# Optimization experiments

Measured on AMD Instinct MI355X. Metric: run time of the kernel, lower is better.

The kernel has to match this reference:

```python
import jax, jax.numpy as jnp
import numpy as np
from jax import lax

IN_CH = 64
OUT_CH = 64
K = 3
CW = 2 * IN_CH + 49  # in_ch_weight = 2*in_ch + MAX_DISPLACEMENT**2 = 177
B = 8


def setup_inputs() -> dict:
    key = jax.random.key(0)
    ks = jax.random.split(key, 14)
    f = lambda k, s, sc: jax.random.normal(k, s, dtype=jnp.float32) * sc
    he5 = lambda cin: (2.0 / (cin * 25)) ** 0.5
    he3 = lambda cin: (2.0 / (cin * 9)) ** 0.5
    return {
        "x0": f(ks[0], (B, IN_CH, 128, 160), 1.0),
        "y0": f(ks[1], (B, IN_CH, 128, 160), 1.0),
        "x": f(ks[2], (B, IN_CH, 64, 80), 1.0),
        "y": f(ks[3], (B, IN_CH, 64, 80), 1.0),
        # weight-branch 0 (outputs CW channels)
        "w1a": f(ks[4], (IN_CH, CW, 5, 5), he5(CW)),
        "w1b": f(ks[5], (IN_CH, IN_CH, 5, 5), he5(IN_CH)),
        "w1c": f(ks[6], (CW, IN_CH, 3, 3), he3(IN_CH)),
        # weight-branch 1 / final (outputs OUT_CH channels)
        "w2a": f(ks[7], (IN_CH, CW, 5, 5), he5(CW)),
        "w2b": f(ks[8], (IN_CH, IN_CH, 5, 5), he5(IN_CH)),
        "w2c": f(ks[9], (OUT_CH, IN_CH, 3, 3), he3(IN_CH)),
        # grouped 1x1 dynamic-weight generators (per-channel affine maps)
        "wx_w": f(ks[10], (CW, CW * K * K), 0.05),
        "wx_b": f(ks[11], (CW, CW * K * K), 0.05),
        "wxf_w": f(ks[12], (OUT_CH, OUT_CH * K * K), 0.05),
        "wxf_b": f(ks[13], (OUT_CH, OUT_CH * K * K), 0.05),
    }


def _conv(x, w, stride, pad):
    return lax.conv_general_dilated(
        x, w, (stride, stride), [(pad, pad), (pad, pad)],
        dimension_numbers=("NCHW", "OIHW", "NCHW"))


def _pool2(x):
    b, c, h, w = x.shape
    return x.reshape(b, c, h // 2, 2, w // 2, 2).mean(axis=(3, 5))


def _corr(x0, y0):
    # FlowNet-style correlation: max_displacement=7, stride2=2 ->
    # displacements {-6,-4,-2,0,2,4,6}^2 = 49 channels; mean over C.
    b, c, h, w = x0.shape
    D = 6
    yp = jnp.pad(y0, ((0, 0), (0, 0), (D, D), (D, D)))
    outs = []
    for dy in range(-6, 7, 2):
        for dx in range(-6, 7, 2):
            ys = yp[:, :, D + dy:D + dy + h, D + dx:D + dx + w]
            outs.append(jnp.mean(x0 * ys, axis=1))
    return jnp.stack(outs, axis=1)  # [B, 49, H, W]


def _branch(feat, wa, wb, wc):
    h = jax.nn.relu(_conv(feat, wa, 2, 2))
    h = jax.nn.relu(_conv(h, wb, 2, 2))
    h = _conv(h, wc, 2, 1)
    return h.mean(axis=(2, 3))  # adaptive_avg_pool2d -> (1,1), squeezed: [B, Cout]


def _adaptive_conv(x, w, pad):
    # per-sample conv weights w: [B, Cout, Cin, k, k]
    def one(xb, wb):
        return _conv(xb[None], wb, 1, pad)[0]
    return jax.vmap(one)(x, w)


def reference(x0, y0, x, y, w1a, w1b, w1c, w2a, w2b, w2c, wx_w, wx_b, wxf_w, wxf_b):
    b = x.shape[0]
    x0p = _pool2(x0)
    y0p = _pool2(y0)
    corr = _corr(x0p, y0p)                      # [B, 49, H, W]
    feat = jnp.concatenate([corr, x, y], axis=1)  # [B, CW, H, W]

    # iteration 0 (N-1 = 1): generate per-sample [CW,CW,3,3] filters, apply
    fv = _branch(feat, w1a, w1b, w1c)           # [B, CW]
    wx = (fv[:, :, None] * wx_w[None] + wx_b[None]).reshape(b, CW, CW, K, K)
    feat = jax.nn.relu(_adaptive_conv(feat, wx, K // 2))

    # final: generate per-sample [OUT_CH,OUT_CH,3,3] filters and return them
    fv = _branch(feat, w2a, w2b, w2c)           # [B, OUT_CH]
    wxf = (fv[:, :, None] * wxf_w[None] + wxf_b[None]).reshape(b, OUT_CH, OUT_CH, K, K)
    return wxf
```

## Files before the change

kernel.cpp:

```cpp
#include <hip/hip_runtime.h>

typedef unsigned short u16;
typedef __attribute__((ext_vector_type(8))) short bf16x8;
typedef __attribute__((ext_vector_type(4))) float f32x4;
typedef _Float16 half2_t __attribute__((ext_vector_type(2)));

static constexpr int B  = 8;
static constexpr int C  = 64;
static constexpr int CW = 177;
static constexpr int H  = 64, W  = 80;
static constexpr int HP = 68, WP = 84, KC = 192;
static constexpr int PB = HP * WP * KC;
static constexpr int HA = 36, WA = 44;

__device__ __forceinline__ u16 f2b(float f) {
  union { float f; unsigned u; } v; v.f = f;
  unsigned u = v.u;
  return (u16)((u + 0x7FFF + ((u >> 16) & 1)) >> 16);
}
__device__ __forceinline__ u16 f2h(float f) {
  union { _Float16 h; u16 u; } v; v.h = (_Float16)f; return v.u;
}
__device__ __forceinline__ half2_t h2(unsigned u) {
  union { unsigned u; half2_t h; } v; v.u = u; return v.h;
}
__device__ __forceinline__ float blo(unsigned u) {
  union { unsigned v; float f; } t; t.v = u << 16; return t.f;
}
__device__ __forceinline__ float bhi(unsigned u) {
  union { unsigned v; float f; } t; t.v = u & 0xffff0000u; return t.f;
}
__device__ __forceinline__ unsigned pk2(u16 a, u16 b) {
  return (unsigned)a | ((unsigned)b << 16);
}

__global__ __launch_bounds__(256) void setup_pool(
    const float* __restrict__ x0, const float* __restrict__ y0,
    u16* __restrict__ xpT, u16* __restrict__ ypT,
    const float* __restrict__ w1a, const float* __restrict__ w2a,
    const float* __restrict__ w1b, const float* __restrict__ w2b,
    u16* __restrict__ A5a, u16* __restrict__ A5b,
    u16* __restrict__ A5b1, u16* __restrict__ A5b2,
    u16* __restrict__ featP1, u16* __restrict__ haP, u16* __restrict__ featP2) {
  __shared__ u16 lt[80][66];
  int blk0 = blockIdx.x;
  int tid = threadIdx.x;
  if (blk0 < 1024) {
    int sel = blk0 & 1; int h = (blk0 >> 1) & 63; int b = blk0 >> 7;
    const float* in = sel ? y0 : x0;
    u16* out = sel ? ypT : xpT;
#pragma unroll
    for (int i = 0; i < 20; ++i) {
      int e = i * 256 + tid;
      int c = e / 80, w = e % 80;
      const float* p = in + ((size_t)(b * 64 + c) * 128 + 2 * h) * 160 + 2 * w;
      float2 r0 = *(const float2*)p;
      float2 r1 = *(const float2*)(p + 160);
      lt[w][c] = f2h(0.25f * (r0.x + r0.y + r1.x + r1.y));
    }
    __syncthreads();
#pragma unroll
    for (int i = 0; i < 20; ++i) {
      int e = i * 256 + tid;
      int w = e / 64, c = e % 64;
      out[((size_t)(b * H + h) * W + w) * C + c] = lt[w][c];
    }
    return;
  }
  int idx = (blk0 - 1024) * 256 + tid;
  const int n0r = (B * PB) / 8;
  const int n1r = (B * HA * WA * 64) / 8;
  const int n2r = B * 592 * 24;
  const int s1 = 25 * 64 * 192, s2 = 25 * 64 * 64;
  bf16x8 z = 0;
  if (idx < n0r) { ((bf16x8*)featP1)[idx] = z; return; }
  idx -= n0r;
  if (idx < n1r) { ((bf16x8*)haP)[idx] = z; return; }
  idx -= n1r;
  if (idx < n2r) {
    int ch = idx % 24; int pi = (idx / 24) % 592; int b = idx / (24 * 592);
    int row, col;
    if (pi < 336) { int rr = pi / 84; row = (rr < 2) ? rr : rr + 64; col = pi % 84; }
    else { int pj = pi - 336; row = 2 + (pj >> 2); int cc = pj & 3; col = (cc < 2) ? cc : cc + 80; }
    *(bf16x8*)(featP2 + ((size_t)(b * HP + row) * WP + col) * KC + ch * 8) = z;
    return;
  }
  idx -= n2r;
  if (idx < 2 * s1) {
    const float* w = idx < s1 ? w1a : w2a; u16* A = idx < s1 ? A5a : A5b;
    int e = idx % s1;
    int j = e % 192; int i = (e / 192) % 64; int kk = e / (192 * 64);
    int ky = kk / 5, kx = kk % 5;
    float v = (j < CW) ? w[(((size_t)i * CW + j) * 5 + ky) * 5 + kx] : 0.f;
    A[e] = f2b(v);
    return;
  }
  idx -= 2 * s1;
  if (idx < 2 * s2) {
    const float* w = idx < s2 ? w1b : w2b; u16* A = idx < s2 ? A5b1 : A5b2;
    int e = idx % s2;
    int j = e % 64; int i = (e / 64) % 64; int kk = e / (64 * 64);
    int ky = kk / 5, kx = kk % 5;
    A[e] = f2b(w[(((size_t)i * 64 + j) * 5 + ky) * 5 + kx]);
  }
}

__global__ __launch_bounds__(256) void corr_copy(
    const u16* __restrict__ xpT, const u16* __restrict__ ypT,
    const float* __restrict__ x, const float* __restrict__ y,
    u16* __restrict__ featP) {
  __shared__ char sm[40960];
  int blk0 = blockIdx.x;
  int tid = threadIdx.x;
  if (blk0 < 512) {
    int b = blk0 & 7; int h = blk0 >> 3;
    const u16* yb = ypT + (size_t)b * (H * W * C);
    uint4 xv[8];
    {
      const u16* xb = xpT + (((size_t)b * H + h) * W + (tid % 80)) * C;
#pragma unroll
      for (int s = 0; s < 8; ++s) xv[s] = *(const uint4*)(xb + s * 8);
    }
    int w = tid % 80; int og = tid / 80;
    u16* dst = featP + ((size_t)(b * HP + h + 2) * WP + (w + 2)) * KC;
#pragma unroll
    for (int ph = 0; ph < 2; ++ph) {
      const int nrows = ph ? 3 : 4;
      const int nch = nrows * 640;
      if (ph) __syncthreads();
      for (int it = 0; it * 256 + tid < nch; ++it) {
        int idx = it * 256 + tid;
        int row = idx / 640; int rem = idx - row * 640; int q = rem >> 3; int slot = rem & 7;
        int hh = h - 6 + 2 * (ph * 4 + row);
        bf16x8 v = 0;
        if (hh >= 0 && hh < H) v = *(const bf16x8*)(yb + ((size_t)hh * W + q) * C + slot * 8);
        int byte = (idx * 16) ^ ((q & 7) << 4);
        *(bf16x8*)(sm + byte) = v;
      }
      __syncthreads();
      if (tid < 240) {
        const int base = ph ? 28 : 0;
        const int cnt = ph ? 7 : 10;
        const int bound = ph ? 49 : 28;
#pragma unroll
        for (int oi = 0; oi < 10; ++oi) {
          if (oi >= cnt) break;
          int o = base + og * cnt + oi;
          if (o < bound) {
            int rr = o / 7; int dx = (o % 7) * 2 - 6;
            int lr = rr - ph * 4;
            int ww = w + dx;
            float s = 0.f;
            if (ww >= 0 && ww < W) {
#pragma unroll
              for (int sl = 0; sl < 8; ++sl) {
                int byte = (((lr * 640) + ww * 8 + sl) * 16) ^ ((ww & 7) << 4);
                uint4 yv = *(const uint4*)(sm + byte);
                s = __builtin_amdgcn_fdot2(h2(xv[sl].x), h2(yv.x), s, false);
                s = __builtin_amdgcn_fdot2(h2(xv[sl].y), h2(yv.y), s, false);
                s = __builtin_amdgcn_fdot2(h2(xv[sl].z), h2(yv.z), s, false);
                s = __builtin_amdgcn_fdot2(h2(xv[sl].w), h2(yv.w), s, false);
              }
            }
            dst[o] = f2b(s * (1.0f / 64.0f));
          }
        }
      }
    }
    return;
  }
  int blk = blk0 - 512;
  float (*lt)[129] = (float(*)[129])sm;
  int half = blk & 1; int h = (blk >> 1) & 63; int b = blk >> 7;
#pragma unroll
  for (int i = 0; i < 20; ++i) {
    int e = i * 256 + tid;
    int c2 = e / 40, w = e % 40;
    const float* src = (c2 < 64) ? x : y;
    int c = c2 & 63;
    lt[w][c2] = src[((size_t)(b * 64 + c) * H + h) * W + half * 40 + w];
  }
  __syncthreads();
#pragma unroll
  for (int i = 0; i < 20; ++i) {
    int e = i * 256 + tid;
    int wr = e / 128, c = e % 128;
    featP[((size_t)(b * HP + h + 2) * WP + (half * 40 + wr + 2)) * KC + 49 + c] = f2b(lt[wr][c]);
  }
}

__global__ void wx_pack(const float* __restrict__ fv, const float* __restrict__ ww,
                        const float* __restrict__ wb, u16* __restrict__ Apk) {
  int idx = blockIdx.x * blockDim.x + threadIdx.x;
  if (idx >= 9 * 192 * 24) return;
  int j8 = idx % 24; int i = (idx / 24) % 192; int kk = idx / (24 * 192);
  float wwv[8], wbv[8];
#pragma unroll
  for (int jj = 0; jj < 8; ++jj) {
    int j = j8 * 8 + jj;
    if (i < CW && j < CW) {
      size_t o = ((size_t)i * CW + j) * 9 + kk;
      wwv[jj] = ww[o]; wbv[jj] = wb[o];
    } else { wwv[jj] = 0.f; wbv[jj] = 0.f; }
  }
  int rb = i >> 4, il = i & 15;
  int c = j8 >> 3, rem = j8 & 7, half = rem >> 2, kqq = rem & 3;
  size_t dst = (((((size_t)kk * 12 + rb) * 3 + c) * 2 + half) * 64 + kqq * 16 + il) * 8;
  for (int b = 0; b < B; ++b) {
    float f = (i < CW) ? fv[b * CW + i] : 0.f;
    u16 o[8];
#pragma unroll
    for (int jj = 0; jj < 8; ++jj) o[jj] = f2b(f * wwv[jj] + wbv[jj]);
    uint4 v; v.x = pk2(o[0], o[1]); v.y = pk2(o[2], o[3]); v.z = pk2(o[4], o[5]); v.w = pk2(o[6], o[7]);
    *(uint4*)(Apk + (size_t)b * 331776 + dst) = v;
  }
}

__global__ __launch_bounds__(256, 2) void ad_conv_kernel(
    const u16* __restrict__ Apk, const u16* __restrict__ featP, u16* __restrict__ outP) {
  __shared__ u16 lds[2][84 * 64];
  int bid = (int)(blockIdx.x % 8) * 64 + (int)(blockIdx.x / 8);
  int h = bid & 63; int b = bid >> 6;
  int tid = threadIdx.x;
  int lane = tid & 63; int wm = tid >> 6;
  int l15 = lane & 15, kq = lane >> 4;

  f32x4 acc[3][5];
#pragma unroll
  for (int i = 0; i < 3; ++i)
#pragma unroll
    for (int j = 0; j < 5; ++j) acc[i][j] = (f32x4){0.f, 0.f, 0.f, 0.f};

  const u16* fb = featP + (size_t)b * PB;
  const u16* Ab = Apk + (size_t)b * 331776 + (size_t)lane * 8;

  int i0 = tid, i1 = tid + 256, i2 = tid + 512;
  int q0 = i0 >> 3, s0 = i0 & 7;
  int q1 = i1 >> 3, s1 = i1 & 7;
  int q2 = i2 >> 3, s2 = i2 & 7;
  int w0 = (i0 * 16) ^ ((q0 & 7) << 4);
  int w1 = (i1 * 16) ^ ((q1 & 7) << 4);
  int w2 = (i2 * 16) ^ ((q2 & 7) << 4);
  bool a2 = i2 < 672;

  bf16x8 r0, r1, r2;
  {
    const u16* g = fb + ((size_t)(h + 1) * WP) * KC;
    r0 = *(const bf16x8*)(g + (size_t)q0 * KC + s0 * 8);
    r1 = *(const bf16x8*)(g + (size_t)q1 * KC + s1 * 8);
    if (a2) r2 = *(const bf16x8*)(g + (size_t)q2 * KC + s2 * 8);
    char* lw = (char*)lds[0];
    *(bf16x8*)(lw + w0) = r0;
    *(bf16x8*)(lw + w1) = r1;
    if (a2) *(bf16x8*)(lw + w2) = r2;
  }
  __syncthreads();

#pragma unroll
  for (int s = 0; s < 9; ++s) {
    const int c = s / 3, ty = s % 3;
    if (s < 8) {
      const int cn = (s + 1) / 3, tyn = (s + 1) % 3;
      const u16* g = fb + ((size_t)(h + 1 + tyn) * WP) * KC + cn * 64;
      r0 = *(const bf16x8*)(g + (size_t)q0 * KC + s0 * 8);
      r1 = *(const bf16x8*)(g + (size_t)q1 * KC + s1 * 8);
      if (a2) r2 = *(const bf16x8*)(g + (size_t)q2 * KC + s2 * 8);
    }
    const char* lb = (const char*)lds[s & 1];
#pragma unroll
    for (int tx = 0; tx < 3; ++tx) {
      const int tap = ty * 3 + tx;
#pragma unroll
      for (int hk = 0; hk < 2; ++hk) {
        bf16x8 av[3], bv[5];
#pragma unroll
        for (int fm = 0; fm < 3; ++fm)
          av[fm] = *(const bf16x8*)(Ab + (size_t)(((tap * 12 + wm * 3 + fm) * 3 + c) * 2 + hk) * 512);
#pragma unroll
        for (int fn = 0; fn < 5; ++fn) {
          int q = fn * 16 + l15 + tx + 1;
          int byte = ((q * 8 + hk * 4 + kq) * 16) ^ ((q & 7) << 4);
          bv[fn] = *(const bf16x8*)(lb + byte);
        }
        __builtin_amdgcn_s_setprio(1);
#pragma unroll
        for (int fm = 0; fm < 3; ++fm)
#pragma unroll
          for (int fn = 0; fn < 5; ++fn)
            acc[fm][fn] = __builtin_amdgcn_mfma_f32_16x16x32_bf16(av[fm], bv[fn], acc[fm][fn], 0, 0, 0);
        __builtin_amdgcn_s_setprio(0);
      }
    }
    if (s < 8) {
      char* lw = (char*)lds[(s + 1) & 1];
      *(bf16x8*)(lw + w0) = r0;
      *(bf16x8*)(lw + w1) = r1;
      if (a2) *(bf16x8*)(lw + w2) = r2;
      __syncthreads();
    }
  }

#pragma unroll
  for (int fm = 0; fm < 3; ++fm) {
    int i0r = wm * 48 + fm * 16 + kq * 4;
#pragma unroll
    for (int fn = 0; fn < 5; ++fn) {
      int ow = fn * 16 + l15;
      u16* dst = outP + ((size_t)(b * HP + h + 2) * WP + (ow + 2)) * KC + i0r;
      uint2 pkv;
      pkv.x = pk2(f2b(fmaxf(acc[fm][fn][0], 0.f)), f2b(fmaxf(acc[fm][fn][1], 0.f)));
      pkv.y = pk2(f2b(fmaxf(acc[fm][fn][2], 0.f)), f2b(fmaxf(acc[fm][fn][3], 0.f)));
      *(uint2*)dst = pkv;
    }
  }
}

__global__ __launch_bounds__(128, 3) void conv5_split_kernel(
    const u16* __restrict__ A5, const u16* __restrict__ featP, u16* __restrict__ pa) {
  __shared__ u16 lds[2][84 * 64];
  int bid = (int)(blockIdx.x % 8) * 160 + (int)(blockIdx.x / 8);
  int rp = bid % 16; int ty = (bid / 16) % 5; int csel = (bid / 80) % 2; int b = bid / 160;
  int r0 = rp * 2;
  int kc0 = csel * 3;
  int tid = threadIdx.x;
  int lane = tid & 63; int wm = tid >> 6;
  int l15 = lane & 15, kq = lane >> 4;

  f32x4 acc[2][5];
#pragma unroll
  for (int i = 0; i < 2; ++i)
#pragma unroll
    for (int j = 0; j < 5; ++j) acc[i][j] = (f32x4){0.f, 0.f, 0.f, 0.f};

  const u16* fb = featP + (size_t)b * PB;
  int rowg0 = 2 * r0 + ty;

  bf16x8 r[6];
  auto load_chunk = [&](int kc) {
#pragma unroll
    for (int it = 0; it < 6; ++it) {
      int idx = it * 128 + tid;
      if (idx < 672) {
        int slot = idx & 3; int q = (idx >> 2) % 84; int row = idx / 336;
        r[it] = *(const bf16x8*)(fb + ((size_t)(rowg0 + 2 * row) * WP + q) * KC + kc * 32 + slot * 8);
      }
    }
  };
  auto write_chunk = [&](int buf) {
    char* lw = (char*)lds[buf];
#pragma unroll
    for (int it = 0; it < 6; ++it) {
      int idx = it * 128 + tid;
      if (idx < 672) {
        int q = (idx >> 2) % 84;
        int byte = (idx * 16) ^ ((q & 7) << 4);
        *(bf16x8*)(lw + byte) = r[it];
      }
    }
  };

  load_chunk(kc0);
  write_chunk(0);
  __syncthreads();

#pragma unroll
  for (int k = 0; k < 3; ++k) {
    int kc = kc0 + k;
    if (k < 2) load_chunk(kc + 1);
    const char* lb = (const char*)lds[k & 1];
#pragma unroll
    for (int tx = 0; tx < 5; ++tx) {
      bf16x8 av[2], bv[5];
#pragma unroll
      for (int fm = 0; fm < 2; ++fm)
        av[fm] = *(const bf16x8*)(A5 + ((size_t)((ty * 5 + tx) * 64 + wm * 32 + fm * 16 + l15)) * 192 + kc * 32 + kq * 8);
#pragma unroll
      for (int fn = 0; fn < 5; ++fn) {
        int p = fn * 16 + l15;
        int orow = p / 40, ocol = p % 40;
        int q = ocol * 2 + tx;
        int byte = (((orow * 84 + q) * 4 + kq) * 16) ^ ((q & 7) << 4);
        bv[fn] = *(const bf16x8*)(lb + byte);
      }
      __builtin_amdgcn_s_setprio(1);
#pragma unroll
      for (int fm = 0; fm < 2; ++fm)
#pragma unroll
        for (int fn = 0; fn < 5; ++fn)
          acc[fm][fn] = __builtin_amdgcn_mfma_f32_16x16x32_bf16(av[fm], bv[fn], acc[fm][fn], 0, 0, 0);
      __builtin_amdgcn_s_setprio(0);
    }
    if (k < 2) {
      write_chunk((k + 1) & 1);
      __syncthreads();
    }
  }
  int slot10 = csel * 5 + ty;
#pragma unroll
  for (int fm = 0; fm < 2; ++fm) {
    int oc0 = wm * 32 + fm * 16 + kq * 4;
#pragma unroll
    for (int fn = 0; fn < 5; ++fn) {
      int p = fn * 16 + l15;
      int orow = r0 + p / 40, ocol = p % 40;
      u16* dst = pa + (((((size_t)slot10 * B + b) * 32 + orow) * 40 + ocol) * 64) + oc0;
      uint2 pkv;
      pkv.x = pk2(f2b(acc[fm][fn][0]), f2b(acc[fm][fn][1]));
      pkv.y = pk2(f2b(acc[fm][fn][2]), f2b(acc[fm][fn][3]));
      *(uint2*)dst = pkv;
    }
  }
}

__global__ void combine10(const u16* __restrict__ pa, u16* __restrict__ haP) {
  int idx = blockIdx.x * blockDim.x + threadIdx.x;
  if (idx >= B * 32 * 40 * 8) return;
  int c8 = idx & 7; int t = idx >> 3;
  int ocol = t % 40; t /= 40; int orow = t % 32; int b = t / 32;
  float s[8];
#pragma unroll
  for (int k = 0; k < 8; ++k) s[k] = 0.f;
#pragma unroll
  for (int sl = 0; sl < 10; ++sl) {
    const u16* p = pa + ((((size_t)sl * B + b) * 32 + orow) * 40 + ocol) * 64 + c8 * 8;
    uint4 v = *(const uint4*)p;
    s[0] += blo(v.x); s[1] += bhi(v.x); s[2] += blo(v.y); s[3] += bhi(v.y);
    s[4] += blo(v.z); s[5] += bhi(v.z); s[6] += blo(v.w); s[7] += bhi(v.w);
  }
  uint4 o;
  o.x = pk2(f2b(fmaxf(s[0], 0.f)), f2b(fmaxf(s[1], 0.f)));
  o.y = pk2(f2b(fmaxf(s[2], 0.f)), f2b(fmaxf(s[3], 0.f)));
  o.z = pk2(f2b(fmaxf(s[4], 0.f)), f2b(fmaxf(s[5], 0.f)));
  o.w = pk2(f2b(fmaxf(s[6], 0.f)), f2b(fmaxf(s[7], 0.f)));
  *(uint4*)(haP + ((size_t)(b * HA + orow + 2) * WA + (ocol + 2)) * 64 + c8 * 8) = o;
}

template<int TY, int TX, int S, int OH, int OW, int M, int BM, int BN, int POFF,
         int KCIN, int HPIN, int WPIN>
__global__ __launch_bounds__(256) void gemm_conv(
    const u16* __restrict__ A, const u16* __restrict__ featP,
    float* __restrict__ outF, int MT, int NT) {
  constexpr int WM = BM / 2, WN = BN / 2, FM = WM / 16, FN = WN / 16;
  constexpr int NKC = KCIN / 32;
  int nwg = gridDim.x;
  int bid = (int)(blockIdx.x % 8) * (nwg / 8) + (int)(blockIdx.x / 8);
  int mt = bid % MT; int rest = bid / MT; int nt = rest % NT; int b = rest / NT;
  int lane = threadIdx.x & 63; int wv = threadIdx.x >> 6;
  int wm = wv >> 1, wn = wv & 1;
  int l15 = lane & 15, kq = lane >> 4;

  f32x4 acc[FM][FN];
#pragma unroll
  for (int i = 0; i < FM; ++i)
#pragma unroll
    for (int j = 0; j < FN; ++j) acc[i][j] = (f32x4){0.f, 0.f, 0.f, 0.f};

  const u16* Abase = A + (size_t)(mt * BM + wm * WM + l15) * KCIN + kq * 8;
  const u16* fb = featP + (size_t)b * (HPIN * WPIN * KCIN) + kq * 8;

  int ohh[FN], oww[FN];
#pragma unroll
  for (int fn = 0; fn < FN; ++fn) {
    int p = nt * BN + wn * WN + fn * 16 + l15;
    ohh[fn] = p / OW; oww[fn] = p % OW;
  }

  for (int kc = 0; kc < NKC; ++kc) {
    for (int ty = 0; ty < TY; ++ty)
      for (int tx = 0; tx < TX; ++tx) {
        const u16* At = Abase + (size_t)((ty * TX + tx) * M) * KCIN + kc * 32;
        bf16x8 av[FM], bv[FN];
#pragma unroll
        for (int fm = 0; fm < FM; ++fm)
          av[fm] = *(const bf16x8*)(At + fm * 16 * KCIN);
#pragma unroll
        for (int fn = 0; fn < FN; ++fn) {
          int hi = ohh[fn] * S + ty + POFF;
          int wi = oww[fn] * S + tx + POFF;
          bv[fn] = *(const bf16x8*)(fb + (size_t)(hi * WPIN + wi) * KCIN + kc * 32);
        }
#pragma unroll
        for (int fm = 0; fm < FM; ++fm)
#pragma unroll
          for (int fn = 0; fn < FN; ++fn)
            acc[fm][fn] = __builtin_amdgcn_mfma_f32_16x16x32_bf16(av[fm], bv[fn], acc[fm][fn], 0, 0, 0);
      }
  }

#pragma unroll
  for (int fm = 0; fm < FM; ++fm) {
    int oc0 = mt * BM + wm * WM + fm * 16 + kq * 4;
#pragma unroll
    for (int fn = 0; fn < FN; ++fn) {
#pragma unroll
      for (int r = 0; r < 4; ++r) {
        float v = fmaxf(acc[fm][fn][r], 0.f);
        outF[(((size_t)b * M + oc0 + r) * OH + ohh[fn]) * OW + oww[fn]] = v;
      }
    }
  }
}

__global__ void tapsum_kernel(const float* __restrict__ hb, float* __restrict__ Sm) {
  int b = blockIdx.x >> 6; int ic = blockIdx.x & 63; int lane = threadIdx.x;
  const float* p = hb + ((size_t)(b * 64 + ic)) * 320;
  float s[9];
#pragma unroll
  for (int t = 0; t < 9; ++t) s[t] = 0.f;
  for (int i = lane; i < 320; i += 64) {
    int ih = i / 20, iw = i % 20;
    float v = p[i];
#pragma unroll
    for (int ky = 0; ky < 3; ++ky) {
      int t2 = ih + 1 - ky;
      if (t2 < 0 || t2 > 14 || (t2 & 1)) continue;
#pragma unroll
      for (int kx = 0; kx < 3; ++kx) {
        int t3 = iw + 1 - kx;
        if (t3 < 0 || t3 > 18 || (t3 & 1)) continue;
        s[ky * 3 + kx] += v;
      }
    }
  }
#pragma unroll
  for (int t = 0; t < 9; ++t)
#pragma unroll
    for (int off = 32; off > 0; off >>= 1) s[t] += __shfl_down(s[t], off);
  if (lane == 0) {
#pragma unroll
    for (int t = 0; t < 9; ++t) Sm[(b * 64 + ic) * 9 + t] = s[t];
  }
}

__global__ void gemv_fv(const float* __restrict__ w3, const float* __restrict__ Sm,
                        float* __restrict__ fv, int OC) {
  int o = blockIdx.x % OC; int b = blockIdx.x / OC; int lane = threadIdx.x;
  const float* wp = w3 + ((size_t)o * 64 + lane) * 9;
  const float* sp = Sm + ((size_t)b * 64 + lane) * 9;
  float acc = 0.f;
#pragma unroll
  for (int t = 0; t < 9; ++t) acc += wp[t] * sp[t];
#pragma unroll
  for (int off = 32; off > 0; off >>= 1) acc += __shfl_down(acc, off);
  if (lane == 0) fv[b * OC + o] = acc * (1.0f / 80.0f);
}

__global__ void gemv_final(const float* __restrict__ w3, const float* __restrict__ Sm,
                           const float* __restrict__ ww, const float* __restrict__ wb,
                           float* __restrict__ out) {
  int o = blockIdx.x & 63; int b = blockIdx.x >> 6; int lane = threadIdx.x;
  const float* wp = w3 + ((size_t)o * 64 + lane) * 9;
  const float* sp = Sm + ((size_t)b * 64 + lane) * 9;
  float acc = 0.f;
#pragma unroll
  for (int t = 0; t < 9; ++t) acc += wp[t] * sp[t];
#pragma unroll
  for (int off = 32; off > 0; off >>= 1) acc += __shfl_down(acc, off);
  float fvv = __shfl(acc, 0) * (1.0f / 80.0f);
  const float* wwp = ww + (size_t)o * 576;
  const float* wbp = wb + (size_t)o * 576;
  float* op = out + ((size_t)(b * 64 + o)) * 576;
#pragma unroll
  for (int k = 0; k < 9; ++k)
    op[k * 64 + lane] = fvv * wwp[k * 64 + lane] + wbp[k * 64 + lane];
}

extern "C" void kernel_launch(void* const* d_in, const int* in_sizes, int n_in,
                              void* d_out, int out_size, void* d_ws, size_t ws_size,
                              hipStream_t stream) {
  const float* x0    = (const float*)d_in[0];
  const float* y0    = (const float*)d_in[1];
  const float* x     = (const float*)d_in[2];
  const float* y     = (const float*)d_in[3];
  const float* w1a   = (const float*)d_in[4];
  const float* w1b   = (const float*)d_in[5];
  const float* w1c   = (const float*)d_in[6];
  const float* w2a   = (const float*)d_in[7];
  const float* w2b   = (const float*)d_in[8];
  const float* w2c   = (const float*)d_in[9];
  const float* wx_w  = (const float*)d_in[10];
  const float* wx_b  = (const float*)d_in[11];
  const float* wxf_w = (const float*)d_in[12];
  const float* wxf_b = (const float*)d_in[13];
  float* out = (float*)d_out;

  char* base = (char*)d_ws;
  size_t off = 0;
  auto take = [&](size_t bytes) -> char* {
    char* p = base + off; off += (bytes + 255) & ~(size_t)255; return p;
  };
  u16*   featP1 = (u16*)take((size_t)B * PB * 2);
  u16*   featP2 = (u16*)take((size_t)B * PB * 2);
  u16*   paAwx  = (u16*)take((size_t)10 * B * 32 * 40 * 64 * 2);
  u16*   pa     = paAwx;
  u16*   Apk    = paAwx;
  u16*   xpT    = paAwx;
  u16*   ypT    = paAwx + (size_t)B * H * W * C;
  u16*   A5a    = (u16*)take((size_t)25 * 64 * 192 * 2);
  u16*   A5b    = (u16*)take((size_t)25 * 64 * 192 * 2);
  u16*   A5b1   = (u16*)take((size_t)25 * 64 * 64 * 2);
  u16*   A5b2   = (u16*)take((size_t)25 * 64 * 64 * 2);
  u16*   haP    = (u16*)take((size_t)B * HA * WA * 64 * 2);
  float* hb     = (float*)take((size_t)B * 64 * 320 * 4);
  float* Sm     = (float*)take((size_t)B * 64 * 9 * 4);
  float* fv1    = (float*)take((size_t)B * CW * 4);
  if (off > ws_size) return;

  const int TB = 256;

  {
    int nsetup = (B * PB) / 8 + (B * HA * WA * 64) / 8 + B * 592 * 24
               + 2 * 25 * 64 * 192 + 2 * 25 * 64 * 64;
    int grid = 1024 + (nsetup + TB - 1) / TB;
    setup_pool<<<grid, TB, 0, stream>>>(x0, y0, xpT, ypT,
        w1a, w2a, w1b, w2b, A5a, A5b, A5b1, A5b2, featP1, haP, featP2);
  }
  corr_copy<<<512 + 1024, TB, 0, stream>>>(xpT, ypT, x, y, featP1);

  conv5_split_kernel<<<1280, 128, 0, stream>>>(A5a, featP1, pa);
  combine10<<<(B * 32 * 40 * 8 + TB - 1) / TB, TB, 0, stream>>>(pa, haP);
  gemm_conv<5, 5, 2, 16, 20, 64, 32, 32, 0, 64, HA, WA>
      <<<160, TB, 0, stream>>>(A5b1, haP, hb, 2, 10);
  tapsum_kernel<<<B * 64, 64, 0, stream>>>(hb, Sm);
  gemv_fv<<<B * CW, 64, 0, stream>>>(w1c, Sm, fv1, CW);

  wx_pack<<<(9 * 192 * 24 + TB - 1) / TB, TB, 0, stream>>>(fv1, wx_w, wx_b, Apk);
  ad_conv_kernel<<<64 * B, 256, 0, stream>>>(Apk, featP1, featP2);

  conv5_split_kernel<<<1280, 128, 0, stream>>>(A5b, featP2, pa);
  combine10<<<(B * 32 * 40 * 8 + TB - 1) / TB, TB, 0, stream>>>(pa, haP);
  gemm_conv<5, 5, 2, 16, 20, 64, 32, 32, 0, 64, HA, WA>
      <<<160, TB, 0, stream>>>(A5b2, haP, hb, 2, 10);
  tapsum_kernel<<<B * 64, 64, 0, stream>>>(hb, Sm);
  gemv_final<<<B * 64, 64, 0, stream>>>(w2c, Sm, wxf_w, wxf_b, out);
}
```

Baseline: 172.7 us.

## Pre-pack conv weights in MFMA fragment order and stage three rows per chunk

Setup now writes the 5x5 conv weights in a fragment-packed layout, so each lane loads its MFMA A-operand as one contiguous 16-byte slice. The adaptive conv now stages all three input rows of a 64-channel chunk into LDS at once, giving 3 sync stages instead of 9, at the cost of a larger LDS footprint. The generic gemm_conv template is replaced by a specialized conv5b kernel using the packed weights. The larger LDS use may reduce occupancy of the adaptive conv.

```diff
diff --git a/kernel.cpp b/kernel.cpp
--- a/kernel.cpp
+++ b/kernel.cpp
@@ -92,7 +92,9 @@
     int j = e % 192; int i = (e / 192) % 64; int kk = e / (192 * 64);
     int ky = kk / 5, kx = kk % 5;
     float v = (j < CW) ? w[(((size_t)i * CW + j) * 5 + ky) * 5 + kx] : 0.f;
-    A[e] = f2b(v);
+    int rg = i >> 4, l15 = i & 15;
+    int kc = j >> 5, r = j & 31, kq = r >> 3, s = r & 7;
+    A[(((size_t)(kk * 4 + rg) * 6 + kc) * 64 + kq * 16 + l15) * 8 + s] = f2b(v);
     return;
   }
   idx -= 2 * s1;
@@ -101,7 +103,10 @@
     int e = idx % s2;
     int j = e % 64; int i = (e / 64) % 64; int kk = e / (64 * 64);
     int ky = kk / 5, kx = kk % 5;
-    A[e] = f2b(w[(((size_t)i * 64 + j) * 5 + ky) * 5 + kx]);
+    float v = w[(((size_t)i * 64 + j) * 5 + ky) * 5 + kx];
+    int rg = i >> 4, l15 = i & 15;
+    int kc = j >> 5, r = j & 31, kq = r >> 3, s = r & 7;
+    A[(((size_t)(kk * 4 + rg) * 2 + kc) * 64 + kq * 16 + l15) * 8 + s] = f2b(v);
   }
 }
 
@@ -218,7 +223,7 @@
 
 __global__ __launch_bounds__(256, 2) void ad_conv_kernel(
     const u16* __restrict__ Apk, const u16* __restrict__ featP, u16* __restrict__ outP) {
-  __shared__ u16 lds[2][84 * 64];
+  __shared__ u16 lds[2][3 * 84 * 64];
   int bid = (int)(blockIdx.x % 8) * 64 + (int)(blockIdx.x / 8);
   int h = bid & 63; int b = bid >> 6;
   int tid = threadIdx.x;
@@ -234,68 +239,67 @@
   const u16* fb = featP + (size_t)b * PB;
   const u16* Ab = Apk + (size_t)b * 331776 + (size_t)lane * 8;
 
-  int i0 = tid, i1 = tid + 256, i2 = tid + 512;
-  int q0 = i0 >> 3, s0 = i0 & 7;
-  int q1 = i1 >> 3, s1 = i1 & 7;
-  int q2 = i2 >> 3, s2 = i2 & 7;
-  int w0 = (i0 * 16) ^ ((q0 & 7) << 4);
-  int w1 = (i1 * 16) ^ ((q1 & 7) << 4);
-  int w2 = (i2 * 16) ^ ((q2 & 7) << 4);
-  bool a2 = i2 < 672;
-
-  bf16x8 r0, r1, r2;
-  {
-    const u16* g = fb + ((size_t)(h + 1) * WP) * KC;
-    r0 = *(const bf16x8*)(g + (size_t)q0 * KC + s0 * 8);
-    r1 = *(const bf16x8*)(g + (size_t)q1 * KC + s1 * 8);
-    if (a2) r2 = *(const bf16x8*)(g + (size_t)q2 * KC + s2 * 8);
-    char* lw = (char*)lds[0];
-    *(bf16x8*)(lw + w0) = r0;
-    *(bf16x8*)(lw + w1) = r1;
-    if (a2) *(bf16x8*)(lw + w2) = r2;
-  }
+  bf16x8 r[8];
+  auto load_c = [&](int c) {
+#pragma unroll
+    for (int it = 0; it < 8; ++it) {
+      int idx = it * 256 + tid;
+      if (idx < 2016) {
+        int row = idx / 672; int rem = idx - row * 672; int q = rem >> 3; int slot = rem & 7;
+        r[it] = *(const bf16x8*)(fb + ((size_t)(h + 1 + row) * WP + q) * KC + c * 64 + slot * 8);
+      }
+    }
+  };
+  auto write_c = [&](int buf) {
+    char* lw = (char*)lds[buf];
+#pragma unroll
+    for (int it = 0; it < 8; ++it) {
+      int idx = it * 256 + tid;
+      if (idx < 2016) {
+        int q = (idx % 672) >> 3;
+        int byte = (idx * 16) ^ ((q & 7) << 4);
+        *(bf16x8*)(lw + byte) = r[it];
+      }
+    }
+  };
+
+  load_c(0);
+  write_c(0);
   __syncthreads();
 
 #pragma unroll
-  for (int s = 0; s < 9; ++s) {
-    const int c = s / 3, ty = s % 3;
-    if (s < 8) {
-      const int cn = (s + 1) / 3, tyn = (s + 1) % 3;
-      const u16* g = fb + ((size_t)(h + 1 + tyn) * WP) * KC + cn * 64;
-      r0 = *(const bf16x8*)(g + (size_t)q0 * KC + s0 * 8);
-      r1 = *(const bf16x8*)(g + (size_t)q1 * KC + s1 * 8);
-      if (a2) r2 = *(const bf16x8*)(g + (size_t)q2 * KC + s2 * 8);
-    }
-    const char* lb = (const char*)lds[s & 1];
-#pragma unroll
-    for (int tx = 0; tx < 3; ++tx) {
-      const int tap = ty * 3 + tx;
-#pragma unroll
-      for (int hk = 0; hk < 2; ++hk) {
-        bf16x8 av[3], bv[5];
-#pragma unroll
-        for (int fm = 0; fm < 3; ++fm)
-          av[fm] = *(const bf16x8*)(Ab + (size_t)(((tap * 12 + wm * 3 + fm) * 3 + c) * 2 + hk) * 512);
-#pragma unroll
-        for (int fn = 0; fn < 5; ++fn) {
-          int q = fn * 16 + l15 + tx + 1;
-          int byte = ((q * 8 + hk * 4 + kq) * 16) ^ ((q & 7) << 4);
-          bv[fn] = *(const bf16x8*)(lb + byte);
+  for (int c = 0; c < 3; ++c) {
+    if (c < 2) load_c(c + 1);
+    const char* lb = (const char*)lds[c & 1];
+#pragma unroll
+    for (int ty = 0; ty < 3; ++ty)
+#pragma unroll
+      for (int tx = 0; tx < 3; ++tx) {
+        const int tap = ty * 3 + tx;
+#pragma unroll
+        for (int hk = 0; hk < 2; ++hk) {
+          bf16x8 av[3], bv[5];
+#pragma unroll
+          for (int fm = 0; fm < 3; ++fm)
+            av[fm] = *(const bf16x8*)(Ab + (size_t)(((tap * 12 + wm * 3 + fm) * 3 + c) * 2 + hk) * 512);
+#pragma unroll
+          for (int fn = 0; fn < 5; ++fn) {
+            int q = fn * 16 + l15 + tx + 1;
+            int idx = ty * 672 + q * 8 + hk * 4 + kq;
+            int byte = (idx * 16) ^ ((q & 7) << 4);
+            bv[fn] = *(const bf16x8*)(lb + byte);
+          }
+          __builtin_amdgcn_s_setprio(1);
+#pragma unroll
+          for (int fm = 0; fm < 3; ++fm)
+#pragma unroll
+            for (int fn = 0; fn < 5; ++fn)
+              acc[fm][fn] = __builtin_amdgcn_mfma_f32_16x16x32_bf16(av[fm], bv[fn], acc[fm][fn], 0, 0, 0);
+          __builtin_amdgcn_s_setprio(0);
         }
-        __builtin_amdgcn_s_setprio(1);
-#pragma unroll
-        for (int fm = 0; fm < 3; ++fm)
-#pragma unroll
-          for (int fn = 0; fn < 5; ++fn)
-            acc[fm][fn] = __builtin_amdgcn_mfma_f32_16x16x32_bf16(av[fm], bv[fn], acc[fm][fn], 0, 0, 0);
-        __builtin_amdgcn_s_setprio(0);
-      }
-    }
-    if (s < 8) {
-      char* lw = (char*)lds[(s + 1) & 1];
-      *(bf16x8*)(lw + w0) = r0;
-      *(bf16x8*)(lw + w1) = r1;
-      if (a2) *(bf16x8*)(lw + w2) = r2;
+      }
+    if (c < 2) {
+      write_c((c + 1) & 1);
       __syncthreads();
     }
   }
@@ -370,10 +374,11 @@
     const char* lb = (const char*)lds[k & 1];
 #pragma unroll
     for (int tx = 0; tx < 5; ++tx) {
+      int tap = ty * 5 + tx;
       bf16x8 av[2], bv[5];
 #pragma unroll
       for (int fm = 0; fm < 2; ++fm)
-        av[fm] = *(const bf16x8*)(A5 + ((size_t)((ty * 5 + tx) * 64 + wm * 32 + fm * 16 + l15)) * 192 + kc * 32 + kq * 8);
+        av[fm] = *(const bf16x8*)(A5 + ((size_t)((tap * 4 + wm * 2 + fm) * 6 + kc)) * 512 + lane * 8);
 #pragma unroll
       for (int fn = 0; fn < 5; ++fn) {
         int p = fn * 16 + l15;
@@ -435,69 +440,37 @@
   *(uint4*)(haP + ((size_t)(b * HA + orow + 2) * WA + (ocol + 2)) * 64 + c8 * 8) = o;
 }
 
-template<int TY, int TX, int S, int OH, int OW, int M, int BM, int BN, int POFF,
-         int KCIN, int HPIN, int WPIN>
-__global__ __launch_bounds__(256) void gemm_conv(
-    const u16* __restrict__ A, const u16* __restrict__ featP,
-    float* __restrict__ outF, int MT, int NT) {
-  constexpr int WM = BM / 2, WN = BN / 2, FM = WM / 16, FN = WN / 16;
-  constexpr int NKC = KCIN / 32;
-  int nwg = gridDim.x;
-  int bid = (int)(blockIdx.x % 8) * (nwg / 8) + (int)(blockIdx.x / 8);
-  int mt = bid % MT; int rest = bid / MT; int nt = rest % NT; int b = rest / NT;
+__global__ __launch_bounds__(256) void conv5b_kernel(
+    const u16* __restrict__ A, const u16* __restrict__ haP, float* __restrict__ outF) {
+  int bid = (int)(blockIdx.x % 8) * 20 + (int)(blockIdx.x / 8);
+  int mt = bid % 2; int nt = (bid / 2) % 10; int b = bid / 20;
   int lane = threadIdx.x & 63; int wv = threadIdx.x >> 6;
   int wm = wv >> 1, wn = wv & 1;
   int l15 = lane & 15, kq = lane >> 4;
 
-  f32x4 acc[FM][FN];
-#pragma unroll
-  for (int i = 0; i < FM; ++i)
-#pragma unroll
-    for (int j = 0; j < FN; ++j) acc[i][j] = (f32x4){0.f, 0.f, 0.f, 0.f};
-
-  const u16* Abase = A + (size_t)(mt * BM + wm * WM + l15) * KCIN + kq * 8;
-  const u16* fb = featP + (size_t)b * (HPIN * WPIN * KCIN) + kq * 8;
-
-  int ohh[FN], oww[FN];
-#pragma unroll
-  for (int fn = 0; fn < FN; ++fn) {
-    int p = nt * BN + wn * WN + fn * 16 + l15;
-    ohh[fn] = p / OW; oww[fn] = p % OW;
-  }
-
-  for (int kc = 0; kc < NKC; ++kc) {
-    for (int ty = 0; ty < TY; ++ty)
-      for (int tx = 0; tx < TX; ++tx) {
-        const u16* At = Abase + (size_t)((ty * TX + tx) * M) * KCIN + kc * 32;
-        bf16x8 av[FM], bv[FN];
-#pragma unroll
-        for (int fm = 0; fm < FM; ++fm)
-          av[fm] = *(const bf16x8*)(At + fm * 16 * KCIN);
-#pragma unroll
-        for (int fn = 0; fn < FN; ++fn) {
-          int hi = ohh[fn] * S + ty + POFF;
-          int wi = oww[fn] * S + tx + POFF;
-          bv[fn] = *(const bf16x8*)(fb + (size_t)(hi * WPIN + wi) * KCIN + kc * 32);
-        }
-#pragma unroll
-        for (int fm = 0; fm < FM; ++fm)
-#pragma unroll
-          for (int fn = 0; fn < FN; ++fn)
-            acc[fm][fn] = __builtin_amdgcn_mfma_f32_16x16x32_bf16(av[fm], bv[fn], acc[fm][fn], 0, 0, 0);
-      }
-  }
-
-#pragma unroll
-  for (int fm = 0; fm < FM; ++fm) {
-    int oc0 = mt * BM + wm * WM + fm * 16 + kq * 4;
-#pragma unroll
-    for (int fn = 0; fn < FN; ++fn) {
-#pragma unroll
-      for (int r = 0; r < 4; ++r) {
-        float v = fmaxf(acc[fm][fn][r], 0.f);
-        outF[(((size_t)b * M + oc0 + r) * OH + ohh[fn]) * OW + oww[fn]] = v;
-      }
-    }
+  f32x4 acc = (f32x4){0.f, 0.f, 0.f, 0.f};
+  int p = nt * 32 + wn * 16 + l15;
+  int oh = p / 20, ow = p % 20;
+  const u16* fb = haP + (size_t)b * (HA * WA * 64) + kq * 8;
+
+  for (int kc = 0; kc < 2; ++kc) {
+#pragma unroll
+    for (int ty = 0; ty < 5; ++ty)
+#pragma unroll
+      for (int tx = 0; tx < 5; ++tx) {
+        int tap = ty * 5 + tx;
+        bf16x8 av = *(const bf16x8*)(A + ((size_t)((tap * 4 + mt * 2 + wm) * 2 + kc)) * 512 + lane * 8);
+        int hi = oh * 2 + ty, wi = ow * 2 + tx;
+        bf16x8 bv = *(const bf16x8*)(fb + (size_t)(hi * WA + wi) * 64 + kc * 32);
+        acc = __builtin_amdgcn_mfma_f32_16x16x32_bf16(av, bv, acc, 0, 0, 0);
+      }
+  }
+
+  int oc0 = mt * 32 + wm * 16 + kq * 4;
+#pragma unroll
+  for (int r = 0; r < 4; ++r) {
+    float v = fmaxf(acc[r], 0.f);
+    outF[(((size_t)b * 64 + oc0 + r) * 16 + oh) * 20 + ow] = v;
   }
 }
 
@@ -619,8 +592,7 @@
 
   conv5_split_kernel<<<1280, 128, 0, stream>>>(A5a, featP1, pa);
   combine10<<<(B * 32 * 40 * 8 + TB - 1) / TB, TB, 0, stream>>>(pa, haP);
-  gemm_conv<5, 5, 2, 16, 20, 64, 32, 32, 0, 64, HA, WA>
-      <<<160, TB, 0, stream>>>(A5b1, haP, hb, 2, 10);
+  conv5b_kernel<<<160, TB, 0, stream>>>(A5b1, haP, hb);
   tapsum_kernel<<<B * 64, 64, 0, stream>>>(hb, Sm);
   gemv_fv<<<B * CW, 64, 0, stream>>>(w1c, Sm, fv1, CW);
 
@@ -629,8 +601,7 @@
 
   conv5_split_kernel<<<1280, 128, 0, stream>>>(A5b, featP2, pa);
   combine10<<<(B * 32 * 40 * 8 + TB - 1) / TB, TB, 0, stream>>>(pa, haP);
-  gemm_conv<5, 5, 2, 16, 20, 64, 32, 32, 0, 64, HA, WA>
-      <<<160, TB, 0, stream>>>(A5b2, haP, hb, 2, 10);
+  conv5b_kernel<<<160, TB, 0, stream>>>(A5b2, haP, hb);
   tapsum_kernel<<<B * 64, 64, 0, stream>>>(hb, Sm);
   gemv_final<<<B * 64, 64, 0, stream>>>(w2c, Sm, wxf_w, wxf_b, out);
 }
```

Result: no change. 172.9 us (+0.2%).
